# Performance work log

Measured on AMD Instinct MI355X. Metric: run time of the kernel, lower is better.

Reference implementation:

```python
import jax, jax.numpy as jnp
import numpy as np

B, S, D, H, O, E = 2, 2048, 1024, 2048, 1024, 8


def setup_inputs() -> dict:
    key = jax.random.key(0)
    k_x, k_rw, k_w1, k_w3, k_w2 = jax.random.split(key, 5)
    sD = 1.0 / np.sqrt(D)
    sH = 1.0 / np.sqrt(H)
    return {
        "x": jax.random.normal(k_x, (B, S, D), dtype=jnp.float32),
        "router_w": jax.random.normal(k_rw, (E, D), dtype=jnp.float32) * sD,  # nn.Linear(D, E).weight
        "router_b": jnp.zeros((E,), dtype=jnp.float32),
        "W1": jax.random.normal(k_w1, (E, D, H), dtype=jnp.float32) * sD,  # per-expert w1 (x @ W1)
        "W3": jax.random.normal(k_w3, (E, D, H), dtype=jnp.float32) * sD,  # per-expert gate w3
        "W2": jax.random.normal(k_w2, (E, H, O), dtype=jnp.float32) * sH,  # per-expert down-proj
        "top_k": 2,
    }


def reference(x, router_w, router_b, W1, W3, W2, top_k):
    b, s, d = x.shape
    xf = x.reshape(-1, d)  # [T, D], T = B*S
    T = xf.shape[0]

    # Router: softmax over experts, then top-k and renormalize
    logits = xf @ router_w.T + router_b            # [T, E]
    probs = jax.nn.softmax(logits, axis=-1)
    top_p, top_i = jax.lax.top_k(probs, top_k)     # [T, k]
    top_p = top_p / top_p.sum(axis=-1, keepdims=True)

    # Dense all-expert SwiGLU MLPs (faithful to reference: every expert on every token)
    h = jnp.einsum('td,edh->eth', xf, W1)          # [E, T, H]
    g = jnp.einsum('td,edh->eth', xf, W3)          # [E, T, H]
    eo = jnp.einsum('eth,eho->eto', jax.nn.silu(h) * g, W2)  # [E, T, O]

    # Gather each token's top-k expert outputs and combine
    sel = eo[top_i, jnp.arange(T)[:, None]]        # [T, k, O]
    out = jnp.sum(top_p[..., None] * sel, axis=1)  # [T, O]
    return out.reshape(b, s, -1)
```

## Files before the change

### kernel.cpp

```cpp
#include <hip/hip_runtime.h>
#include <hip/hip_bf16.h>

#define TTOK 4096
#define DIM  1024
#define HID  2048
#define ODIM 1024
#define NE   8

typedef __attribute__((ext_vector_type(8))) short  short8;
typedef __attribute__((ext_vector_type(4))) float  f32x4;
typedef __attribute__((ext_vector_type(8))) unsigned short ushort8;

__device__ __forceinline__ unsigned short f2bf(float f){
  unsigned u = __float_as_uint(f);
  u += 0x7fffu + ((u >> 16) & 1u);
  return (unsigned short)(u >> 16);
}

__device__ __forceinline__ void gld16(const void* g, void* l){
  __builtin_amdgcn_global_load_lds(
      (const __attribute__((address_space(1))) unsigned int*)g,
      (__attribute__((address_space(3))) unsigned int*)l, 16, 0, 0);
}

__global__ __launch_bounds__(256) void router_kernel(
    const float* __restrict__ x, const float* __restrict__ rw,
    const float* __restrict__ rb, unsigned short* __restrict__ xbf,
    int2* __restrict__ toke, float2* __restrict__ tokw)
{
  int tok  = (blockIdx.x * blockDim.x + threadIdx.x) >> 6;
  int lane = threadIdx.x & 63;
  const float4* xr = (const float4*)(x + (size_t)tok * DIM + lane * 16);
  float xv[16];
#pragma unroll
  for (int q = 0; q < 4; q++){
    float4 v = xr[q];
    xv[q*4+0]=v.x; xv[q*4+1]=v.y; xv[q*4+2]=v.z; xv[q*4+3]=v.w;
  }
  ushort8 u0, u1;
#pragma unroll
  for (int j = 0; j < 8; j++){ u0[j] = f2bf(xv[j]); u1[j] = f2bf(xv[8+j]); }
  ushort8* xo = (ushort8*)(xbf + (size_t)tok * DIM + lane * 16);
  xo[0] = u0; xo[1] = u1;

  float lg[NE];
#pragma unroll
  for (int e = 0; e < NE; e++){
    const float4* wr4 = (const float4*)(rw + (size_t)e * DIM + lane * 16);
    float s = 0.f;
#pragma unroll
    for (int q = 0; q < 4; q++){
      float4 wv = wr4[q];
      s += xv[q*4+0]*wv.x + xv[q*4+1]*wv.y + xv[q*4+2]*wv.z + xv[q*4+3]*wv.w;
    }
    lg[e] = s;
  }
#pragma unroll
  for (int e = 0; e < NE; e++)
    for (int s = 1; s < 64; s <<= 1) lg[e] += __shfl_xor(lg[e], s, 64);

  if (lane == 0){
#pragma unroll
    for (int e = 0; e < NE; e++) lg[e] += rb[e];
    int e0 = 0; float l0 = lg[0];
    for (int e = 1; e < NE; e++) if (lg[e] > l0){ l0 = lg[e]; e0 = e; }
    int e1 = -1; float l1 = -1e30f;
    for (int e = 0; e < NE; e++) if (e != e0 && lg[e] > l1){ l1 = lg[e]; e1 = e; }
    float w0 = 1.f / (1.f + __expf(l1 - l0));
    float w1 = 1.f / (1.f + __expf(l0 - l1));
    toke[tok] = make_int2(e0, e1);
    tokw[tok] = make_float2(w0, w1);
  }
}

__global__ __launch_bounds__(256) void plan_kernel(
    const int2* __restrict__ toke, const float2* __restrict__ tokw,
    int* __restrict__ counts, int* __restrict__ offs,
    int* __restrict__ tlist, float* __restrict__ wlist)
{
  const int e  = blockIdx.x;
  const int t  = threadIdx.x;
  const int lane = t & 63, wv = t >> 6;
  __shared__ int sh[4 * 8];
  __shared__ int tot[8];
  __shared__ int sw[4];

  int wcnt[NE];
#pragma unroll
  for (int ee = 0; ee < NE; ee++) wcnt[ee] = 0;
  for (int base = 0; base < TTOK; base += 256){
    int2 p = toke[base + t];
#pragma unroll
    for (int ee = 0; ee < NE; ee++){
      unsigned long long m = __ballot(p.x == ee || p.y == ee);
      if (lane == 0) wcnt[ee] += __popcll(m);
    }
  }
  if (lane == 0){
#pragma unroll
    for (int ee = 0; ee < NE; ee++) sh[wv * 8 + ee] = wcnt[ee];
  }
  __syncthreads();
  if (t < NE) tot[t] = sh[t] + sh[8 + t] + sh[16 + t] + sh[24 + t];
  __syncthreads();

  int my_off = 0;
#pragma unroll
  for (int ee = 0; ee < NE; ee++) if (ee < e) my_off += tot[ee];

  if (e == 0 && t < NE){
    counts[t] = tot[t];
    int o = 0;
    for (int ee = 0; ee < NE; ee++){ if (ee < t) o += tot[ee]; }
    offs[t] = o;
    if (t == 0){
      int s = 0;
      for (int ee = 0; ee < NE; ee++) s += tot[ee];
      offs[NE] = s;
    }
  }

  int running = my_off;
  for (int base = 0; base < TTOK; base += 256){
    int tokid = base + t;
    int2  p = toke[tokid];
    float2 wgt = tokw[tokid];
    bool s0 = (p.x == e), s1 = (p.y == e);
    bool flag = s0 || s1;
    unsigned long long m = __ballot(flag);
    int rank_in_wave = __popcll(m & ((lane == 0) ? 0ull : ((~0ull) >> (64 - lane))));
    if (lane == 0) sw[wv] = __popcll(m);
    __syncthreads();
    int wave_base = 0, tot4 = 0;
#pragma unroll
    for (int w2 = 0; w2 < 4; w2++){ int v = sw[w2]; tot4 += v; if (w2 < wv) wave_base += v; }
    if (flag){
      int pos = running + wave_base + rank_in_wave;
      tlist[pos] = tokid;
      wlist[pos] = s0 ? wgt.x : wgt.y;
    }
    running += tot4;
    __syncthreads();
  }
}

__global__ __launch_bounds__(256) void transpose_cvt(
    const float* __restrict__ in, unsigned short* __restrict__ out, int R, int C)
{
  __shared__ __align__(16) unsigned short tl[64 * 128];
  int e = blockIdx.z;
  const float* src = in + (size_t)e * R * C + (size_t)(blockIdx.y * 128) * C + blockIdx.x * 64;
  unsigned short* dst = out + (size_t)e * C * R + (size_t)(blockIdx.x * 64) * R + blockIdx.y * 128;
  int t = threadIdx.x;
#pragma unroll
  for (int i = 0; i < 8; i++){
    int idx = i * 256 + t;
    int c = idx & 63, r0 = (idx >> 6) * 4;
    unsigned short v[4];
#pragma unroll
    for (int j = 0; j < 4; j++) v[j] = f2bf(src[(size_t)(r0 + j) * C + c]);
    unsigned long long pk = (unsigned long long)v[0] | ((unsigned long long)v[1] << 16)
      | ((unsigned long long)v[2] << 32) | ((unsigned long long)v[3] << 48);
    *(unsigned long long*)((char*)tl + c * 256 + (((r0 >> 3) ^ (c & 15)) * 16) + (r0 & 7) * 2) = pk;
  }
  __syncthreads();
#pragma unroll
  for (int i = 0; i < 4; i++){
    int idx = i * 256 + t;
    int c = idx >> 4, r0 = (idx & 15) * 8;
    ushort8 u = *(const ushort8*)((const char*)tl + c * 256 + (((r0 >> 3) ^ (c & 15)) * 16));
    *(ushort8*)(dst + (size_t)c * R + r0) = u;
  }
}

__global__ __launch_bounds__(256,2) void ffn1_kernel(
    const unsigned short* __restrict__ xbf,
    const unsigned short* __restrict__ w1t,
    const unsigned short* __restrict__ w3t,
    unsigned short* __restrict__ abuf,
    const int* __restrict__ counts, const int* __restrict__ offs,
    const int* __restrict__ tlist)
{
  const int e = blockIdx.x, ct = blockIdx.y, rt = blockIdx.z;
  const int cnt = counts[e];
  const int rbase = rt * 128;
  if (rbase >= cnt) return;
  const int off = offs[e];
  const int rows_left = cnt - rbase;
  const int t = threadIdx.x;
  const int lane = t & 63, w = t >> 6;
  const int wr = w >> 1, wc = w & 1;

  __shared__ __align__(16) unsigned short lds[2 * 12288];

  int ar0 = t >> 2, ar1 = 64 + (t >> 2);
  int psw = (t & 3) ^ ((t >> 3) & 3);
  int ra0 = ar0 < rows_left ? ar0 : rows_left - 1;
  int ra1 = ar1 < rows_left ? ar1 : rows_left - 1;
  int tok0 = tlist[off + rbase + ra0];
  int tok1 = tlist[off + rbase + ra1];
  const char* sA0  = (const char*)xbf + ((size_t)tok0 * DIM) * 2 + psw * 16;
  const char* sA1  = (const char*)xbf + ((size_t)tok1 * DIM) * 2 + psw * 16;
  const char* sB10 = (const char*)w1t + (((size_t)e * HID + ct * 128 + ar0) * DIM) * 2 + psw * 16;
  const char* sB11 = (const char*)w1t + (((size_t)e * HID + ct * 128 + ar1) * DIM) * 2 + psw * 16;
  const char* sB30 = (const char*)w3t + (((size_t)e * HID + ct * 128 + ar0) * DIM) * 2 + psw * 16;
  const char* sB31 = (const char*)w3t + (((size_t)e * HID + ct * 128 + ar1) * DIM) * 2 + psw * 16;
  const int dofs = w * 1024;

  auto STAGE = [&](int bs, int kt){
    int kb = kt << 6;
    char* base = (char*)lds + bs * 24576;
    gld16(sA0  + kb, base +            dofs);
    gld16(sA1  + kb, base +  4096 +    dofs);
    gld16(sB10 + kb, base +  8192 +    dofs);
    gld16(sB11 + kb, base + 12288 +    dofs);
    gld16(sB30 + kb, base + 16384 +    dofs);
    gld16(sB31 + kb, base + 20480 +    dofs);
  };

  const int chsw = ((lane >> 4) ^ ((lane >> 1) & 3)) * 8;
  int aofs[4], b1ofs[4], b3ofs[4];
#pragma unroll
  for (int i = 0; i < 4; i++){
    int am = wr * 64 + i * 16 + (lane & 15);
    int bn = wc * 64 + i * 16 + (lane & 15);
    aofs[i]  = am * 32 + chsw;
    b1ofs[i] = 4096 + bn * 32 + chsw;
    b3ofs[i] = 8192 + bn * 32 + chsw;
  }

  f32x4 acch[4][4], accg[4][4];
#pragma unroll
  for (int i = 0; i < 4; i++)
#pragma unroll
    for (int j = 0; j < 4; j++){
      acch[i][j] = (f32x4){0.f,0.f,0.f,0.f};
      accg[i][j] = (f32x4){0.f,0.f,0.f,0.f};
    }

  STAGE(0, 0);
  __syncthreads();
#pragma unroll 2
  for (int kt = 0; kt + 1 < DIM / 32; ++kt){
    const int bs = kt & 1;
    STAGE(bs ^ 1, kt + 1);
    const unsigned short* L = lds + bs * 12288;
    short8 a[4], b1[4], b3[4];
#pragma unroll
    for (int i = 0; i < 4; i++){
      a[i]  = *(const short8*)(L + aofs[i]);
      b1[i] = *(const short8*)(L + b1ofs[i]);
      b3[i] = *(const short8*)(L + b3ofs[i]);
    }
#pragma unroll
    for (int mi = 0; mi < 4; mi++)
#pragma unroll
      for (int ni = 0; ni < 4; ni++){
        acch[mi][ni] = __builtin_amdgcn_mfma_f32_16x16x32_bf16(a[mi], b1[ni], acch[mi][ni], 0, 0, 0);
        accg[mi][ni] = __builtin_amdgcn_mfma_f32_16x16x32_bf16(a[mi], b3[ni], accg[mi][ni], 0, 0, 0);
      }
    __syncthreads();
  }
  {
    const int bs = (DIM / 32 - 1) & 1;
    const unsigned short* L = lds + bs * 12288;
    short8 a[4], b1[4], b3[4];
#pragma unroll
    for (int i = 0; i < 4; i++){
      a[i]  = *(const short8*)(L + aofs[i]);
      b1[i] = *(const short8*)(L + b1ofs[i]);
      b3[i] = *(const short8*)(L + b3ofs[i]);
    }
#pragma unroll
    for (int mi = 0; mi < 4; mi++)
#pragma unroll
      for (int ni = 0; ni < 4; ni++){
        acch[mi][ni] = __builtin_amdgcn_mfma_f32_16x16x32_bf16(a[mi], b1[ni], acch[mi][ni], 0, 0, 0);
        accg[mi][ni] = __builtin_amdgcn_mfma_f32_16x16x32_bf16(a[mi], b3[ni], accg[mi][ni], 0, 0, 0);
      }
  }

#pragma unroll
  for (int mi = 0; mi < 4; mi++)
#pragma unroll
    for (int r = 0; r < 4; r++){
      int row_local = wr * 64 + mi * 16 + ((lane >> 4) << 2) + r;
      if (row_local < rows_left){
        size_t pair = (size_t)(off + rbase + row_local);
        unsigned short* arow = abuf + pair * HID + ct * 128 + wc * 64 + (lane & 15);
#pragma unroll
        for (int ni = 0; ni < 4; ni++){
          float h = acch[mi][ni][r], g = accg[mi][ni][r];
          float sv = h / (1.f + __expf(-h));
          arow[ni * 16] = f2bf(sv * g);
        }
      }
    }
}

__global__ __launch_bounds__(256,2) void ffn2_kernel(
    const unsigned short* __restrict__ abuf,
    const unsigned short* __restrict__ w2t,
    float* __restrict__ dout,
    const int* __restrict__ counts, const int* __restrict__ offs,
    const int* __restrict__ tlist, const float* __restrict__ wlist)
{
  const int e = blockIdx.x, ct = blockIdx.y, rt = blockIdx.z;
  const int cnt = counts[e];
  const int rbase = rt * 128;
  if (rbase >= cnt) return;
  const int off = offs[e];
  const int rows_left = cnt - rbase;
  const int t = threadIdx.x;
  const int lane = t & 63, w = t >> 6;
  const int wr = w >> 1, wc = w & 1;

  __shared__ __align__(16) unsigned short lds[2 * 8192];

  int ar0 = t >> 2, ar1 = 64 + (t >> 2);
  int psw = (t & 3) ^ ((t >> 3) & 3);
  int ra0 = ar0 < rows_left ? ar0 : rows_left - 1;
  int ra1 = ar1 < rows_left ? ar1 : rows_left - 1;
  const char* sA0 = (const char*)abuf + ((size_t)(off + rbase + ra0) * HID) * 2 + psw * 16;
  const char* sA1 = (const char*)abuf + ((size_t)(off + rbase + ra1) * HID) * 2 + psw * 16;
  const char* sB0 = (const char*)w2t + (((size_t)e * ODIM + ct * 128 + ar0) * HID) * 2 + psw * 16;
  const char* sB1 = (const char*)w2t + (((size_t)e * ODIM + ct * 128 + ar1) * HID) * 2 + psw * 16;
  const int dofs = w * 1024;

  auto STAGE = [&](int bs, int kt){
    int kb = kt << 6;
    char* base = (char*)lds + bs * 16384;
    gld16(sA0 + kb, base +           dofs);
    gld16(sA1 + kb, base +  4096 +   dofs);
    gld16(sB0 + kb, base +  8192 +   dofs);
    gld16(sB1 + kb, base + 12288 +   dofs);
  };

  const int chsw = ((lane >> 4) ^ ((lane >> 1) & 3)) * 8;
  int aofs[4], bofs[4];
#pragma unroll
  for (int i = 0; i < 4; i++){
    int am = wr * 64 + i * 16 + (lane & 15);
    int bn = wc * 64 + i * 16 + (lane & 15);
    aofs[i] = am * 32 + chsw;
    bofs[i] = 4096 + bn * 32 + chsw;
  }

  f32x4 acc[4][4];
#pragma unroll
  for (int i = 0; i < 4; i++)
#pragma unroll
    for (int j = 0; j < 4; j++) acc[i][j] = (f32x4){0.f,0.f,0.f,0.f};

  STAGE(0, 0);
  __syncthreads();
#pragma unroll 2
  for (int kt = 0; kt + 1 < HID / 32; ++kt){
    const int bs = kt & 1;
    STAGE(bs ^ 1, kt + 1);
    const unsigned short* L = lds + bs * 8192;
    short8 a[4], b[4];
#pragma unroll
    for (int i = 0; i < 4; i++){
      a[i] = *(const short8*)(L + aofs[i]);
      b[i] = *(const short8*)(L + bofs[i]);
    }
#pragma unroll
    for (int mi = 0; mi < 4; mi++)
#pragma unroll
      for (int ni = 0; ni < 4; ni++)
        acc[mi][ni] = __builtin_amdgcn_mfma_f32_16x16x32_bf16(a[mi], b[ni], acc[mi][ni], 0, 0, 0);
    __syncthreads();
  }
  {
    const int bs = (HID / 32 - 1) & 1;
    const unsigned short* L = lds + bs * 8192;
    short8 a[4], b[4];
#pragma unroll
    for (int i = 0; i < 4; i++){
      a[i] = *(const short8*)(L + aofs[i]);
      b[i] = *(const short8*)(L + bofs[i]);
    }
#pragma unroll
    for (int mi = 0; mi < 4; mi++)
#pragma unroll
      for (int ni = 0; ni < 4; ni++)
        acc[mi][ni] = __builtin_amdgcn_mfma_f32_16x16x32_bf16(a[mi], b[ni], acc[mi][ni], 0, 0, 0);
  }

#pragma unroll
  for (int mi = 0; mi < 4; mi++)
#pragma unroll
    for (int r = 0; r < 4; r++){
      int row_local = wr * 64 + mi * 16 + ((lane >> 4) << 2) + r;
      if (row_local < rows_left){
        int pair = off + rbase + row_local;
        int token = tlist[pair];
        float p   = wlist[pair];
        float* orow = dout + (size_t)token * ODIM + ct * 128 + wc * 64 + (lane & 15);
#pragma unroll
        for (int ni = 0; ni < 4; ni++)
          atomicAdd(orow + ni * 16, p * acc[mi][ni][r]);
      }
    }
}

extern "C" void kernel_launch(void* const* d_in, const int* in_sizes, int n_in,
                              void* d_out, int out_size, void* d_ws, size_t ws_size,
                              hipStream_t stream)
{
  const float* x  = (const float*)d_in[0];
  const float* rw = (const float*)d_in[1];
  const float* rb = (const float*)d_in[2];
  const float* W1 = (const float*)d_in[3];
  const float* W3 = (const float*)d_in[4];
  const float* W2 = (const float*)d_in[5];

  char* ws = (char*)d_ws;
  const size_t off_ctrl = 0;
  const size_t off_toke = 256;
  const size_t off_tokw = off_toke + (size_t)TTOK * 8;
  const size_t off_tl   = off_tokw + (size_t)TTOK * 8;
  const size_t off_wl   = off_tl   + (size_t)2 * TTOK * 4;
  const size_t off_xbf  = off_wl   + (size_t)2 * TTOK * 4;
  const size_t off_w1t  = off_xbf  + (size_t)TTOK * DIM * 2;
  const size_t off_w3t  = off_w1t  + (size_t)NE * HID * DIM * 2;
  const size_t off_w2t  = off_w3t  + (size_t)NE * HID * DIM * 2;
  const size_t off_ab   = off_w2t  + (size_t)NE * ODIM * HID * 2;
  const size_t need     = off_ab   + (size_t)2 * TTOK * HID * 2;
  if (ws_size < need) return;

  int* counts = (int*)(ws + off_ctrl);
  int* offs   = (int*)(ws + off_ctrl + 64);
  int2*   toke = (int2*)  (ws + off_toke);
  float2* tokw = (float2*)(ws + off_tokw);
  int*    tl   = (int*)   (ws + off_tl);
  float*  wl   = (float*) (ws + off_wl);
  unsigned short* xbf = (unsigned short*)(ws + off_xbf);
  unsigned short* w1t = (unsigned short*)(ws + off_w1t);
  unsigned short* w3t = (unsigned short*)(ws + off_w3t);
  unsigned short* w2t = (unsigned short*)(ws + off_w2t);
  unsigned short* ab  = (unsigned short*)(ws + off_ab);

  hipMemsetAsync(d_out, 0, (size_t)out_size * sizeof(float), stream);

  router_kernel<<<TTOK / 4, 256, 0, stream>>>(x, rw, rb, xbf, toke, tokw);
  plan_kernel<<<NE, 256, 0, stream>>>(toke, tokw, counts, offs, tl, wl);

  transpose_cvt<<<dim3(HID / 64, DIM / 128, NE), 256, 0, stream>>>(W1, w1t, DIM, HID);
  transpose_cvt<<<dim3(HID / 64, DIM / 128, NE), 256, 0, stream>>>(W3, w3t, DIM, HID);
  transpose_cvt<<<dim3(ODIM / 64, HID / 128, NE), 256, 0, stream>>>(W2, w2t, HID, ODIM);

  ffn1_kernel<<<dim3(NE, HID / 128, 32), 256, 0, stream>>>(xbf, w1t, w3t, ab, counts, offs, tl);
  ffn2_kernel<<<dim3(NE, ODIM / 128, 32), 256, 0, stream>>>(ab, w2t, (float*)d_out, counts, offs, tl, wl);
}
```

Baseline: 252.0 us.

## Triple-buffer LDS in both FFN GEMMs with explicit vmcnt waits and setprio

Both expert GEMM kernels move from a double-buffered LDS loop with __syncthreads to a three-stage ring. Two tiles stay in flight via global_load_lds while one is computed, and completion is tracked with explicit s_waitcnt vmcnt counts plus raw s_barrier. MFMA sections are wrapped in s_setprio to favour the math waves, and ffn2 asks for 3 blocks per CU. The goal is to hide more global-load latency. The cost is more LDS per block, which may lower occupancy for ffn1, and the hand-counted vmcnt values must match the number of loads each STAGE issues.

```diff
diff --git a/kernel.cpp b/kernel.cpp
--- a/kernel.cpp
+++ b/kernel.cpp
@@ -10,6 +10,9 @@
 typedef __attribute__((ext_vector_type(8))) short  short8;
 typedef __attribute__((ext_vector_type(4))) float  f32x4;
 typedef __attribute__((ext_vector_type(8))) unsigned short ushort8;
+
+#define WAITVM(N) asm volatile("s_waitcnt vmcnt(" #N ")" ::: "memory")
+#define BAR() __builtin_amdgcn_s_barrier()
 
 __device__ __forceinline__ unsigned short f2bf(float f){
   unsigned u = __float_as_uint(f);
@@ -191,7 +194,7 @@
   const int lane = t & 63, w = t >> 6;
   const int wr = w >> 1, wc = w & 1;
 
-  __shared__ __align__(16) unsigned short lds[2 * 12288];
+  __shared__ __align__(16) unsigned short lds[3 * 12288];
 
   int ar0 = t >> 2, ar1 = 64 + (t >> 2);
   int psw = (t & 3) ^ ((t >> 3) & 3);
@@ -238,12 +241,7 @@
       accg[i][j] = (f32x4){0.f,0.f,0.f,0.f};
     }
 
-  STAGE(0, 0);
-  __syncthreads();
-#pragma unroll 2
-  for (int kt = 0; kt + 1 < DIM / 32; ++kt){
-    const int bs = kt & 1;
-    STAGE(bs ^ 1, kt + 1);
+  auto COMPUTE = [&](int bs){
     const unsigned short* L = lds + bs * 12288;
     short8 a[4], b1[4], b3[4];
 #pragma unroll
@@ -252,6 +250,7 @@
       b1[i] = *(const short8*)(L + b1ofs[i]);
       b3[i] = *(const short8*)(L + b3ofs[i]);
     }
+    __builtin_amdgcn_s_setprio(1);
 #pragma unroll
     for (int mi = 0; mi < 4; mi++)
 #pragma unroll
@@ -259,26 +258,21 @@
         acch[mi][ni] = __builtin_amdgcn_mfma_f32_16x16x32_bf16(a[mi], b1[ni], acch[mi][ni], 0, 0, 0);
         accg[mi][ni] = __builtin_amdgcn_mfma_f32_16x16x32_bf16(a[mi], b3[ni], accg[mi][ni], 0, 0, 0);
       }
-    __syncthreads();
-  }
-  {
-    const int bs = (DIM / 32 - 1) & 1;
-    const unsigned short* L = lds + bs * 12288;
-    short8 a[4], b1[4], b3[4];
-#pragma unroll
-    for (int i = 0; i < 4; i++){
-      a[i]  = *(const short8*)(L + aofs[i]);
-      b1[i] = *(const short8*)(L + b1ofs[i]);
-      b3[i] = *(const short8*)(L + b3ofs[i]);
-    }
-#pragma unroll
-    for (int mi = 0; mi < 4; mi++)
-#pragma unroll
-      for (int ni = 0; ni < 4; ni++){
-        acch[mi][ni] = __builtin_amdgcn_mfma_f32_16x16x32_bf16(a[mi], b1[ni], acch[mi][ni], 0, 0, 0);
-        accg[mi][ni] = __builtin_amdgcn_mfma_f32_16x16x32_bf16(a[mi], b3[ni], accg[mi][ni], 0, 0, 0);
-      }
-  }
+    __builtin_amdgcn_s_setprio(0);
+  };
+
+  STAGE(0, 0); STAGE(1, 1); STAGE(2, 2);
+  int cur = 0;
+  for (int kt = 0; kt < DIM / 32 - 3; ++kt){
+    WAITVM(12); BAR();
+    COMPUTE(cur);
+    BAR();
+    STAGE(cur, kt + 3);
+    cur = (cur == 2) ? 0 : cur + 1;
+  }
+  WAITVM(12); BAR(); COMPUTE(cur); BAR(); cur = (cur == 2) ? 0 : cur + 1;
+  WAITVM(6);  BAR(); COMPUTE(cur); BAR(); cur = (cur == 2) ? 0 : cur + 1;
+  WAITVM(0);  BAR(); COMPUTE(cur);
 
 #pragma unroll
   for (int mi = 0; mi < 4; mi++)
@@ -298,7 +292,7 @@
     }
 }
 
-__global__ __launch_bounds__(256,2) void ffn2_kernel(
+__global__ __launch_bounds__(256,3) void ffn2_kernel(
     const unsigned short* __restrict__ abuf,
     const unsigned short* __restrict__ w2t,
     float* __restrict__ dout,
@@ -315,7 +309,7 @@
   const int lane = t & 63, w = t >> 6;
   const int wr = w >> 1, wc = w & 1;
 
-  __shared__ __align__(16) unsigned short lds[2 * 8192];
+  __shared__ __align__(16) unsigned short lds[3 * 8192];
 
   int ar0 = t >> 2, ar1 = 64 + (t >> 2);
   int psw = (t & 3) ^ ((t >> 3) & 3);
@@ -352,12 +346,7 @@
 #pragma unroll
     for (int j = 0; j < 4; j++) acc[i][j] = (f32x4){0.f,0.f,0.f,0.f};
 
-  STAGE(0, 0);
-  __syncthreads();
-#pragma unroll 2
-  for (int kt = 0; kt + 1 < HID / 32; ++kt){
-    const int bs = kt & 1;
-    STAGE(bs ^ 1, kt + 1);
+  auto COMPUTE = [&](int bs){
     const unsigned short* L = lds + bs * 8192;
     short8 a[4], b[4];
 #pragma unroll
@@ -365,28 +354,27 @@
       a[i] = *(const short8*)(L + aofs[i]);
       b[i] = *(const short8*)(L + bofs[i]);
     }
+    __builtin_amdgcn_s_setprio(1);
 #pragma unroll
     for (int mi = 0; mi < 4; mi++)
 #pragma unroll
       for (int ni = 0; ni < 4; ni++)
         acc[mi][ni] = __builtin_amdgcn_mfma_f32_16x16x32_bf16(a[mi], b[ni], acc[mi][ni], 0, 0, 0);
-    __syncthreads();
-  }
-  {
-    const int bs = (HID / 32 - 1) & 1;
-    const unsigned short* L = lds + bs * 8192;
-    short8 a[4], b[4];
-#pragma unroll
-    for (int i = 0; i < 4; i++){
-      a[i] = *(const short8*)(L + aofs[i]);
-      b[i] = *(const short8*)(L + bofs[i]);
-    }
-#pragma unroll
-    for (int mi = 0; mi < 4; mi++)
-#pragma unroll
-      for (int ni = 0; ni < 4; ni++)
-        acc[mi][ni] = __builtin_amdgcn_mfma_f32_16x16x32_bf16(a[mi], b[ni], acc[mi][ni], 0, 0, 0);
-  }
+    __builtin_amdgcn_s_setprio(0);
+  };
+
+  STAGE(0, 0); STAGE(1, 1); STAGE(2, 2);
+  int cur = 0;
+  for (int kt = 0; kt < HID / 32 - 3; ++kt){
+    WAITVM(8); BAR();
+    COMPUTE(cur);
+    BAR();
+    STAGE(cur, kt + 3);
+    cur = (cur == 2) ? 0 : cur + 1;
+  }
+  WAITVM(8); BAR(); COMPUTE(cur); BAR(); cur = (cur == 2) ? 0 : cur + 1;
+  WAITVM(4); BAR(); COMPUTE(cur); BAR(); cur = (cur == 2) ? 0 : cur + 1;
+  WAITVM(0); BAR(); COMPUTE(cur);
 
 #pragma unroll
   for (int mi = 0; mi < 4; mi++)
```

Measured after the change: 253.8 us. About the same (+0.7%).

## Interleave W1/W3 weights and enlarge ffn1 tile to 256x256 with 512 threads

Applied to the files above, without the earlier changes.

The W1 and W3 transposes now write into one concatenated weight buffer, interleaved in 16-row groups. This lets ffn1 treat the gate and up projections as a single GEMM with a 256-wide N tile. ffn1 moves to 512 threads with 256-row token tiles and 8x4 MFMA accumulators per wave, which raises reuse of the gathered activation rows per LDS load. The prefetch loop now uses explicit vmcnt waits, raw barriers and s_setprio around the MFMA block. The cost is more LDS per block (64KB) and more accumulator registers, which may limit occupancy, plus coarser row tiles that waste more work on partial tiles.

```diff
diff --git a/kernel.cpp b/kernel.cpp
--- a/kernel.cpp
+++ b/kernel.cpp
@@ -10,6 +10,9 @@
 typedef __attribute__((ext_vector_type(8))) short  short8;
 typedef __attribute__((ext_vector_type(4))) float  f32x4;
 typedef __attribute__((ext_vector_type(8))) unsigned short ushort8;
+
+#define WAITVM(N) asm volatile("s_waitcnt vmcnt(" #N ")" ::: "memory")
+#define BAR() __builtin_amdgcn_s_barrier()
 
 __device__ __forceinline__ unsigned short f2bf(float f){
   unsigned u = __float_as_uint(f);
@@ -145,12 +148,12 @@
 }
 
 __global__ __launch_bounds__(256) void transpose_cvt(
-    const float* __restrict__ in, unsigned short* __restrict__ out, int R, int C)
+    const float* __restrict__ in, unsigned short* __restrict__ out,
+    int R, int C, int ilv, size_t ostride)
 {
   __shared__ __align__(16) unsigned short tl[64 * 128];
   int e = blockIdx.z;
   const float* src = in + (size_t)e * R * C + (size_t)(blockIdx.y * 128) * C + blockIdx.x * 64;
-  unsigned short* dst = out + (size_t)e * C * R + (size_t)(blockIdx.x * 64) * R + blockIdx.y * 128;
   int t = threadIdx.x;
 #pragma unroll
   for (int i = 0; i < 8; i++){
@@ -169,17 +172,110 @@
     int idx = i * 256 + t;
     int c = idx >> 4, r0 = (idx & 15) * 8;
     ushort8 u = *(const ushort8*)((const char*)tl + c * 256 + (((r0 >> 3) ^ (c & 15)) * 16));
-    *(ushort8*)(dst + (size_t)c * R + r0) = u;
-  }
-}
-
-__global__ __launch_bounds__(256,2) void ffn1_kernel(
+    int cg = blockIdx.x * 64 + c;
+    int q  = (ilv < 0) ? cg : (((cg >> 4) << 5) + ilv + (cg & 15));
+    *(ushort8*)(out + (size_t)e * ostride + (size_t)q * R + blockIdx.y * 128 + r0) = u;
+  }
+}
+
+__global__ __launch_bounds__(512,2) void ffn1_kernel(
     const unsigned short* __restrict__ xbf,
-    const unsigned short* __restrict__ w1t,
-    const unsigned short* __restrict__ w3t,
+    const unsigned short* __restrict__ wcat,
     unsigned short* __restrict__ abuf,
     const int* __restrict__ counts, const int* __restrict__ offs,
     const int* __restrict__ tlist)
+{
+  const int e = blockIdx.x, ct = blockIdx.y, rt = blockIdx.z;
+  const int cnt = counts[e];
+  const int rbase = rt * 256;
+  if (rbase >= cnt) return;
+  const int off = offs[e];
+  const int rows_left = cnt - rbase;
+  const int t = threadIdx.x;
+  const int l = t & 63, w = t >> 6;
+  const int wr = w >> 2, wc = w & 3;
+
+  __shared__ __align__(16) unsigned short lds[2 * 16384];
+
+  const int R0 = 32 * w + (l >> 2), R1 = R0 + 16;
+  const int csrc = ((l & 3) ^ ((l >> 3) & 3)) * 16;
+  int raa0 = R0 < rows_left ? R0 : rows_left - 1;
+  int raa1 = R1 < rows_left ? R1 : rows_left - 1;
+  const char* pA0 = (const char*)xbf + (size_t)tlist[off + rbase + raa0] * 2048 + csrc;
+  const char* pA1 = (const char*)xbf + (size_t)tlist[off + rbase + raa1] * 2048 + csrc;
+  const char* pB0 = (const char*)wcat + ((size_t)e * 4096 + ct * 256 + R0) * 2048 + csrc;
+  const char* pB1 = (const char*)wcat + ((size_t)e * 4096 + ct * 256 + R1) * 2048 + csrc;
+
+  auto STAGE = [&](int bs, int kt){
+    int kb = kt << 6;
+    char* base = (char*)lds + bs * 32768;
+    char* d = base + (2 * w) * 1024;
+    gld16(pA0 + kb, d);            gld16(pA1 + kb, d + 1024);
+    gld16(pB0 + kb, d + 16384);    gld16(pB1 + kb, d + 16384 + 1024);
+  };
+
+  const int chsw = ((l >> 4) ^ ((l >> 1) & 3)) * 8;
+  int aro[8], bro[4];
+#pragma unroll
+  for (int mi = 0; mi < 8; mi++) aro[mi] = (wr * 128 + mi * 16 + (l & 15)) * 32 + chsw;
+#pragma unroll
+  for (int ni = 0; ni < 4; ni++) bro[ni] = 8192 + (wc * 64 + ni * 16 + (l & 15)) * 32 + chsw;
+
+  f32x4 acc[8][4];
+#pragma unroll
+  for (int i = 0; i < 8; i++)
+#pragma unroll
+    for (int jj = 0; jj < 4; jj++) acc[i][jj] = (f32x4){0.f,0.f,0.f,0.f};
+
+  auto COMPUTE = [&](int bs){
+    const unsigned short* L = lds + bs * 16384;
+    short8 a[8], b[4];
+#pragma unroll
+    for (int i = 0; i < 8; i++) a[i] = *(const short8*)(L + aro[i]);
+#pragma unroll
+    for (int i = 0; i < 4; i++) b[i] = *(const short8*)(L + bro[i]);
+    __builtin_amdgcn_s_setprio(1);
+#pragma unroll
+    for (int mi = 0; mi < 8; mi++)
+#pragma unroll
+      for (int ni = 0; ni < 4; ni++)
+        acc[mi][ni] = __builtin_amdgcn_mfma_f32_16x16x32_bf16(a[mi], b[ni], acc[mi][ni], 0, 0, 0);
+    __builtin_amdgcn_s_setprio(0);
+  };
+
+  const int NK = DIM / 32;
+  STAGE(0, 0);
+  for (int kt = 0; kt < NK - 1; ++kt){
+    STAGE((kt + 1) & 1, kt + 1);
+    WAITVM(4); BAR();
+    COMPUTE(kt & 1);
+    BAR();
+  }
+  WAITVM(0); BAR();
+  COMPUTE((NK - 1) & 1);
+
+#pragma unroll
+  for (int mi = 0; mi < 8; mi++)
+#pragma unroll
+    for (int r = 0; r < 4; r++){
+      int row_local = wr * 128 + mi * 16 + ((l >> 4) << 2) + r;
+      if (row_local < rows_left){
+        size_t pair = (size_t)(off + rbase + row_local);
+        unsigned short* arow = abuf + pair * HID + ct * 128 + wc * 32 + (l & 15);
+        float h0 = acc[mi][0][r], g0 = acc[mi][1][r];
+        arow[0]  = f2bf((h0 / (1.f + __expf(-h0))) * g0);
+        float h1 = acc[mi][2][r], g1 = acc[mi][3][r];
+        arow[16] = f2bf((h1 / (1.f + __expf(-h1))) * g1);
+      }
+    }
+}
+
+__global__ __launch_bounds__(256,2) void ffn2_kernel(
+    const unsigned short* __restrict__ abuf,
+    const unsigned short* __restrict__ w2t,
+    float* __restrict__ dout,
+    const int* __restrict__ counts, const int* __restrict__ offs,
+    const int* __restrict__ tlist, const float* __restrict__ wlist)
 {
   const int e = blockIdx.x, ct = blockIdx.y, rt = blockIdx.z;
   const int cnt = counts[e];
@@ -191,130 +287,6 @@
   const int lane = t & 63, w = t >> 6;
   const int wr = w >> 1, wc = w & 1;
 
-  __shared__ __align__(16) unsigned short lds[2 * 12288];
-
-  int ar0 = t >> 2, ar1 = 64 + (t >> 2);
-  int psw = (t & 3) ^ ((t >> 3) & 3);
-  int ra0 = ar0 < rows_left ? ar0 : rows_left - 1;
-  int ra1 = ar1 < rows_left ? ar1 : rows_left - 1;
-  int tok0 = tlist[off + rbase + ra0];
-  int tok1 = tlist[off + rbase + ra1];
-  const char* sA0  = (const char*)xbf + ((size_t)tok0 * DIM) * 2 + psw * 16;
-  const char* sA1  = (const char*)xbf + ((size_t)tok1 * DIM) * 2 + psw * 16;
-  const char* sB10 = (const char*)w1t + (((size_t)e * HID + ct * 128 + ar0) * DIM) * 2 + psw * 16;
-  const char* sB11 = (const char*)w1t + (((size_t)e * HID + ct * 128 + ar1) * DIM) * 2 + psw * 16;
-  const char* sB30 = (const char*)w3t + (((size_t)e * HID + ct * 128 + ar0) * DIM) * 2 + psw * 16;
-  const char* sB31 = (const char*)w3t + (((size_t)e * HID + ct * 128 + ar1) * DIM) * 2 + psw * 16;
-  const int dofs = w * 1024;
-
-  auto STAGE = [&](int bs, int kt){
-    int kb = kt << 6;
-    char* base = (char*)lds + bs * 24576;
-    gld16(sA0  + kb, base +            dofs);
-    gld16(sA1  + kb, base +  4096 +    dofs);
-    gld16(sB10 + kb, base +  8192 +    dofs);
-    gld16(sB11 + kb, base + 12288 +    dofs);
-    gld16(sB30 + kb, base + 16384 +    dofs);
-    gld16(sB31 + kb, base + 20480 +    dofs);
-  };
-
-  const int chsw = ((lane >> 4) ^ ((lane >> 1) & 3)) * 8;
-  int aofs[4], b1ofs[4], b3ofs[4];
-#pragma unroll
-  for (int i = 0; i < 4; i++){
-    int am = wr * 64 + i * 16 + (lane & 15);
-    int bn = wc * 64 + i * 16 + (lane & 15);
-    aofs[i]  = am * 32 + chsw;
-    b1ofs[i] = 4096 + bn * 32 + chsw;
-    b3ofs[i] = 8192 + bn * 32 + chsw;
-  }
-
-  f32x4 acch[4][4], accg[4][4];
-#pragma unroll
-  for (int i = 0; i < 4; i++)
-#pragma unroll
-    for (int j = 0; j < 4; j++){
-      acch[i][j] = (f32x4){0.f,0.f,0.f,0.f};
-      accg[i][j] = (f32x4){0.f,0.f,0.f,0.f};
-    }
-
-  STAGE(0, 0);
-  __syncthreads();
-#pragma unroll 2
-  for (int kt = 0; kt + 1 < DIM / 32; ++kt){
-    const int bs = kt & 1;
-    STAGE(bs ^ 1, kt + 1);
-    const unsigned short* L = lds + bs * 12288;
-    short8 a[4], b1[4], b3[4];
-#pragma unroll
-    for (int i = 0; i < 4; i++){
-      a[i]  = *(const short8*)(L + aofs[i]);
-      b1[i] = *(const short8*)(L + b1ofs[i]);
-      b3[i] = *(const short8*)(L + b3ofs[i]);
-    }
-#pragma unroll
-    for (int mi = 0; mi < 4; mi++)
-#pragma unroll
-      for (int ni = 0; ni < 4; ni++){
-        acch[mi][ni] = __builtin_amdgcn_mfma_f32_16x16x32_bf16(a[mi], b1[ni], acch[mi][ni], 0, 0, 0);
-        accg[mi][ni] = __builtin_amdgcn_mfma_f32_16x16x32_bf16(a[mi], b3[ni], accg[mi][ni], 0, 0, 0);
-      }
-    __syncthreads();
-  }
-  {
-    const int bs = (DIM / 32 - 1) & 1;
-    const unsigned short* L = lds + bs * 12288;
-    short8 a[4], b1[4], b3[4];
-#pragma unroll
-    for (int i = 0; i < 4; i++){
-      a[i]  = *(const short8*)(L + aofs[i]);
-      b1[i] = *(const short8*)(L + b1ofs[i]);
-      b3[i] = *(const short8*)(L + b3ofs[i]);
-    }
-#pragma unroll
-    for (int mi = 0; mi < 4; mi++)
-#pragma unroll
-      for (int ni = 0; ni < 4; ni++){
-        acch[mi][ni] = __builtin_amdgcn_mfma_f32_16x16x32_bf16(a[mi], b1[ni], acch[mi][ni], 0, 0, 0);
-        accg[mi][ni] = __builtin_amdgcn_mfma_f32_16x16x32_bf16(a[mi], b3[ni], accg[mi][ni], 0, 0, 0);
-      }
-  }
-
-#pragma unroll
-  for (int mi = 0; mi < 4; mi++)
-#pragma unroll
-    for (int r = 0; r < 4; r++){
-      int row_local = wr * 64 + mi * 16 + ((lane >> 4) << 2) + r;
-      if (row_local < rows_left){
-        size_t pair = (size_t)(off + rbase + row_local);
-        unsigned short* arow = abuf + pair * HID + ct * 128 + wc * 64 + (lane & 15);
-#pragma unroll
-        for (int ni = 0; ni < 4; ni++){
-          float h = acch[mi][ni][r], g = accg[mi][ni][r];
-          float sv = h / (1.f + __expf(-h));
-          arow[ni * 16] = f2bf(sv * g);
-        }
-      }
-    }
-}
-
-__global__ __launch_bounds__(256,2) void ffn2_kernel(
-    const unsigned short* __restrict__ abuf,
-    const unsigned short* __restrict__ w2t,
-    float* __restrict__ dout,
-    const int* __restrict__ counts, const int* __restrict__ offs,
-    const int* __restrict__ tlist, const float* __restrict__ wlist)
-{
-  const int e = blockIdx.x, ct = blockIdx.y, rt = blockIdx.z;
-  const int cnt = counts[e];
-  const int rbase = rt * 128;
-  if (rbase >= cnt) return;
-  const int off = offs[e];
-  const int rows_left = cnt - rbase;
-  const int t = threadIdx.x;
-  const int lane = t & 63, w = t >> 6;
-  const int wr = w >> 1, wc = w & 1;
-
   __shared__ __align__(16) unsigned short lds[2 * 8192];
 
   int ar0 = t >> 2, ar1 = 64 + (t >> 2);
@@ -350,7 +322,7 @@
 #pragma unroll
   for (int i = 0; i < 4; i++)
 #pragma unroll
-    for (int j = 0; j < 4; j++) acc[i][j] = (f32x4){0.f,0.f,0.f,0.f};
+    for (int jj = 0; jj < 4; jj++) acc[i][jj] = (f32x4){0.f,0.f,0.f,0.f};
 
   STAGE(0, 0);
   __syncthreads();
@@ -423,9 +395,8 @@
   const size_t off_tl   = off_tokw + (size_t)TTOK * 8;
   const size_t off_wl   = off_tl   + (size_t)2 * TTOK * 4;
   const size_t off_xbf  = off_wl   + (size_t)2 * TTOK * 4;
-  const size_t off_w1t  = off_xbf  + (size_t)TTOK * DIM * 2;
-  const size_t off_w3t  = off_w1t  + (size_t)NE * HID * DIM * 2;
-  const size_t off_w2t  = off_w3t  + (size_t)NE * HID * DIM * 2;
+  const size_t off_wcat = off_xbf  + (size_t)TTOK * DIM * 2;
+  const size_t off_w2t  = off_wcat + (size_t)NE * 2 * HID * DIM * 2;
   const size_t off_ab   = off_w2t  + (size_t)NE * ODIM * HID * 2;
   const size_t need     = off_ab   + (size_t)2 * TTOK * HID * 2;
   if (ws_size < need) return;
@@ -436,21 +407,20 @@
   float2* tokw = (float2*)(ws + off_tokw);
   int*    tl   = (int*)   (ws + off_tl);
   float*  wl   = (float*) (ws + off_wl);
-  unsigned short* xbf = (unsigned short*)(ws + off_xbf);
-  unsigned short* w1t = (unsigned short*)(ws + off_w1t);
-  unsigned short* w3t = (unsigned short*)(ws + off_w3t);
-  unsigned short* w2t = (unsigned short*)(ws + off_w2t);
-  unsigned short* ab  = (unsigned short*)(ws + off_ab);
+  unsigned short* xbf  = (unsigned short*)(ws + off_xbf);
+  unsigned short* wcat = (unsigned short*)(ws + off_wcat);
+  unsigned short* w2t  = (unsigned short*)(ws + off_w2t);
+  unsigned short* ab   = (unsigned short*)(ws + off_ab);
 
   hipMemsetAsync(d_out, 0, (size_t)out_size * sizeof(float), stream);
 
   router_kernel<<<TTOK / 4, 256, 0, stream>>>(x, rw, rb, xbf, toke, tokw);
   plan_kernel<<<NE, 256, 0, stream>>>(toke, tokw, counts, offs, tl, wl);
 
-  transpose_cvt<<<dim3(HID / 64, DIM / 128, NE), 256, 0, stream>>>(W1, w1t, DIM, HID);
-  transpose_cvt<<<dim3(HID / 64, DIM / 128, NE), 256, 0, stream>>>(W3, w3t, DIM, HID);
-  transpose_cvt<<<dim3(ODIM / 64, HID / 128, NE), 256, 0, stream>>>(W2, w2t, HID, ODIM);
-
-  ffn1_kernel<<<dim3(NE, HID / 128, 32), 256, 0, stream>>>(xbf, w1t, w3t, ab, counts, offs, tl);
+  transpose_cvt<<<dim3(HID / 64, DIM / 128, NE), 256, 0, stream>>>(W1, wcat, DIM, HID, 0,  (size_t)2 * HID * DIM);
+  transpose_cvt<<<dim3(HID / 64, DIM / 128, NE), 256, 0, stream>>>(W3, wcat, DIM, HID, 16, (size_t)2 * HID * DIM);
+  transpose_cvt<<<dim3(ODIM / 64, HID / 128, NE), 256, 0, stream>>>(W2, w2t, HID, ODIM, -1, (size_t)ODIM * HID);
+
+  ffn1_kernel<<<dim3(NE, HID / 128, 32), 512, 0, stream>>>(xbf, wcat, ab, counts, offs, tl);
   ffn2_kernel<<<dim3(NE, ODIM / 128, 32), 256, 0, stream>>>(ab, w2t, (float*)d_out, counts, offs, tl, wl);
 }
```

After: 257.6 us. +2.2%, slower.
